# Optimization experiments

Measured on AMD Instinct MI355X. Metric: run time of the kernel, lower is better.

Reference implementation:

```python
import jax, jax.numpy as jnp
import numpy as np

N_NODES = 50000
N_EDGES = 800000
IN_FEAT = 512
OUT_FEAT = 128


def multispike(x):
    return jnp.floor(jnp.clip(4.0 * x, 0.0, 4.0) + 0.5) / 4.0


def setup_inputs() -> dict:
    key = jax.random.key(0)
    k1, k2, k3, k4, k5 = jax.random.split(key, 5)
    feat = jax.random.normal(k1, (N_NODES, IN_FEAT), dtype=jnp.float32)
    # Xavier-uniform-like init for the weight parameter
    limit = np.sqrt(6.0 / (IN_FEAT + OUT_FEAT)).astype(np.float32)
    weight = jax.random.uniform(k2, (IN_FEAT, OUT_FEAT), dtype=jnp.float32,
                                minval=-limit, maxval=limit)
    rows = jnp.sort(jax.random.randint(k3, (N_EDGES,), 0, N_NODES, dtype=jnp.int32))
    cols = jax.random.randint(k4, (N_EDGES,), 0, N_NODES, dtype=jnp.int32)
    edge_weight = jax.random.uniform(k5, (N_EDGES,), dtype=jnp.float32)
    return {"feat": feat, "weight": weight, "rows": rows, "cols": cols,
            "edge_weight": edge_weight}


def reference(feat, weight, rows, cols, edge_weight):
    # x = feat @ W                     [N, out_feat]
    x = jnp.matmul(feat, weight)
    # x = spmm(adj, x): out[i] = sum_{e: rows[e]==i} w_e * x[cols[e]]
    edge_feats = edge_weight[:, None] * x[cols]          # [E, out_feat]
    x = jax.ops.segment_sum(edge_feats, rows, num_segments=N_NODES)
    # quantized multi-spike activation
    return multispike(x)
```

## Files before the change

### kernel.cpp

```cpp
#include <hip/hip_runtime.h>

#define N_NODES 50000
#define N_EDGES 800000
#define IN_FEAT 512
#define OUT_FEAT 128


__device__ __forceinline__ float multispike(float a) {
    return floorf(fminf(fmaxf(4.0f * a, 0.0f), 4.0f) + 0.5f) * 0.25f;
}

__device__ __forceinline__ int bswz(int q) { return q ^ ((q >> 3) & 1); }

__global__ __launch_bounds__(128) void gemm_kernel(const float* __restrict__ A,
                                                   const float* __restrict__ B,
                                                   float* __restrict__ C, int M) {
    __shared__ float As[32][68];
    __shared__ float Bs[32][128];

    const int tid = threadIdx.x;
    const int tx = tid & 15;
    const int ty = tid >> 4;
    const int block_m = blockIdx.x * 64;

    const int bq0 = bswz(2 * tx) * 4;
    const int bq1 = bswz(2 * tx + 1) * 4;

    float acc[8][8];
#pragma unroll
    for (int i = 0; i < 8; i++)
#pragma unroll
        for (int j = 0; j < 8; j++) acc[i][j] = 0.0f;

    for (int k0 = 0; k0 < IN_FEAT; k0 += 32) {
#pragma unroll
        for (int i = 0; i < 4; i++) {
            int f = tid + i * 128;
            int r = f >> 3;
            int kq = (f & 7) << 2;
            int gm = block_m + r;
            float4 v = make_float4(0.f, 0.f, 0.f, 0.f);
            if (gm < M) v = *(const float4*)(A + (size_t)gm * IN_FEAT + k0 + kq);
            As[kq + 0][r] = v.x;
            As[kq + 1][r] = v.y;
            As[kq + 2][r] = v.z;
            As[kq + 3][r] = v.w;
        }
#pragma unroll
        for (int i = 0; i < 8; i++) {
            int f = tid + i * 128;
            int r = f >> 5;
            int q = f & 31;
            *(float4*)&Bs[r][bswz(q) * 4] =
                *(const float4*)(B + (size_t)(k0 + r) * OUT_FEAT + q * 4);
        }
        __syncthreads();

#pragma unroll
        for (int k = 0; k < 32; k++) {
            float4 a0 = *(const float4*)&As[k][ty * 8];
            float4 a1 = *(const float4*)&As[k][ty * 8 + 4];
            float4 b0 = *(const float4*)&Bs[k][bq0];
            float4 b1 = *(const float4*)&Bs[k][bq1];
            float av[8] = {a0.x, a0.y, a0.z, a0.w, a1.x, a1.y, a1.z, a1.w};
            float bv[8] = {b0.x, b0.y, b0.z, b0.w, b1.x, b1.y, b1.z, b1.w};
#pragma unroll
            for (int i = 0; i < 8; i++)
#pragma unroll
                for (int j = 0; j < 8; j++)
                    acc[i][j] = fmaf(av[i], bv[j], acc[i][j]);
        }
        __syncthreads();
    }

#pragma unroll
    for (int i = 0; i < 8; i++) {
        int gm = block_m + ty * 8 + i;
        if (gm < M) {
            float* cp = C + (size_t)gm * OUT_FEAT + tx * 8;
            *(float4*)cp = make_float4(acc[i][0], acc[i][1], acc[i][2], acc[i][3]);
            *(float4*)(cp + 4) = make_float4(acc[i][4], acc[i][5], acc[i][6], acc[i][7]);
        }
    }
}

__global__ __launch_bounds__(256) void rowptr_kernel(const int* __restrict__ rows,
                                                     int* __restrict__ row_ptr) {
    int i = blockIdx.x * blockDim.x + threadIdx.x;
    if (i > N_NODES) return;
    int lo = 0, hi = N_EDGES;
    while (lo < hi) {
        int mid = (lo + hi) >> 1;
        if (rows[mid] < i) lo = mid + 1; else hi = mid;
    }
    row_ptr[i] = lo;
}

__global__ __launch_bounds__(256) void spmm_kernel(const float* __restrict__ x,
                                                   const int* __restrict__ cols,
                                                   const float* __restrict__ ew,
                                                   const int* __restrict__ row_ptr,
                                                   float* __restrict__ out) {
    const int wave = threadIdx.x >> 6;
    const int lane = threadIdx.x & 63;
    const int r = blockIdx.x * 4 + wave;
    if (r >= N_NODES) return;

    const int e0 = row_ptr[r];
    const int e1 = row_ptr[r + 1];
    const float2* __restrict__ x2 = (const float2*)x;

    float accx = 0.0f, accy = 0.0f;
    int e = e0;
    for (; e + 8 <= e1; e += 8) {
        int c[8];
        float w[8];
        float2 v[8];
#pragma unroll
        for (int j = 0; j < 8; j++) {
            c[j] = cols[e + j];
            w[j] = ew[e + j];
        }
#pragma unroll
        for (int j = 0; j < 8; j++) {
            v[j] = x2[(size_t)c[j] * 64 + lane];
        }
#pragma unroll
        for (int j = 0; j < 8; j++) {
            accx = fmaf(w[j], v[j].x, accx);
            accy = fmaf(w[j], v[j].y, accy);
        }
    }
    for (; e < e1; e++) {
        int c = cols[e];
        float w = ew[e];
        float2 v = x2[(size_t)c * 64 + lane];
        accx = fmaf(w, v.x, accx);
        accy = fmaf(w, v.y, accy);
    }
    float2* out2 = (float2*)out;
    out2[(size_t)r * 64 + lane] = make_float2(multispike(accx), multispike(accy));
}

extern "C" void kernel_launch(void* const* d_in, const int* in_sizes, int n_in,
                              void* d_out, int out_size, void* d_ws, size_t ws_size,
                              hipStream_t stream) {
    const float* feat = (const float*)d_in[0];
    const float* weight = (const float*)d_in[1];
    const int* rows = (const int*)d_in[2];
    const int* cols = (const int*)d_in[3];
    const float* ew = (const float*)d_in[4];
    float* out = (float*)d_out;

    float* x = (float*)d_ws;
    int* row_ptr = (int*)((char*)d_ws + (size_t)N_NODES * OUT_FEAT * sizeof(float));

    rowptr_kernel<<<(N_NODES + 256) / 256, 256, 0, stream>>>(rows, row_ptr);
    gemm_kernel<<<(N_NODES + 63) / 64, 128, 0, stream>>>(feat, weight, x, N_NODES);
    spmm_kernel<<<(N_NODES + 3) / 4, 256, 0, stream>>>(x, cols, ew, row_ptr, out);
}
```

Measured before the change: 316.2 us.

## Replace shared-memory tiled GEMM with wave-per-16-rows register GEMM using uniform A loads

Rewrites the dense feat@W GEMM so that each wave computes 16 output rows. Each lane holds two output columns, B is read straight from global memory as float2, and the A row values are wave-uniform float4 loads that can become scalar loads. This removes the shared-memory staging, the transposed stores and the __syncthreads barriers. In exchange B is re-read from L2/L1 by every wave and each FMA has much less register-level reuse than the old 8x8 tile, so the kernel may become bound by load issue or latency.

```diff
diff --git a/kernel.cpp b/kernel.cpp
--- a/kernel.cpp
+++ b/kernel.cpp
@@ -10,77 +10,51 @@
     return floorf(fminf(fmaxf(4.0f * a, 0.0f), 4.0f) + 0.5f) * 0.25f;
 }
 
-__device__ __forceinline__ int bswz(int q) { return q ^ ((q >> 3) & 1); }
-
-__global__ __launch_bounds__(128) void gemm_kernel(const float* __restrict__ A,
+__global__ __launch_bounds__(256) void gemm_kernel(const float* __restrict__ A,
                                                    const float* __restrict__ B,
                                                    float* __restrict__ C, int M) {
-    __shared__ float As[32][68];
-    __shared__ float Bs[32][128];
+    const int lane = threadIdx.x & 63;
+    const int wv = __builtin_amdgcn_readfirstlane(threadIdx.x >> 6);
+    const int row0 = blockIdx.x * 64 + wv * 16;
 
-    const int tid = threadIdx.x;
-    const int tx = tid & 15;
-    const int ty = tid >> 4;
-    const int block_m = blockIdx.x * 64;
+    const float2* __restrict__ B2 = (const float2*)B;
 
-    const int bq0 = bswz(2 * tx) * 4;
-    const int bq1 = bswz(2 * tx + 1) * 4;
-
-    float acc[8][8];
+    const float* Ar[16];
 #pragma unroll
-    for (int i = 0; i < 8; i++)
-#pragma unroll
-        for (int j = 0; j < 8; j++) acc[i][j] = 0.0f;
-
-    for (int k0 = 0; k0 < IN_FEAT; k0 += 32) {
-#pragma unroll
-        for (int i = 0; i < 4; i++) {
-            int f = tid + i * 128;
-            int r = f >> 3;
-            int kq = (f & 7) << 2;
-            int gm = block_m + r;
-            float4 v = make_float4(0.f, 0.f, 0.f, 0.f);
-            if (gm < M) v = *(const float4*)(A + (size_t)gm * IN_FEAT + k0 + kq);
-            As[kq + 0][r] = v.x;
-            As[kq + 1][r] = v.y;
-            As[kq + 2][r] = v.z;
-            As[kq + 3][r] = v.w;
-        }
-#pragma unroll
-        for (int i = 0; i < 8; i++) {
-            int f = tid + i * 128;
-            int r = f >> 5;
-            int q = f & 31;
-            *(float4*)&Bs[r][bswz(q) * 4] =
-                *(const float4*)(B + (size_t)(k0 + r) * OUT_FEAT + q * 4);
-        }
-        __syncthreads();
-
-#pragma unroll
-        for (int k = 0; k < 32; k++) {
-            float4 a0 = *(const float4*)&As[k][ty * 8];
-            float4 a1 = *(const float4*)&As[k][ty * 8 + 4];
-            float4 b0 = *(const float4*)&Bs[k][bq0];
-            float4 b1 = *(const float4*)&Bs[k][bq1];
-            float av[8] = {a0.x, a0.y, a0.z, a0.w, a1.x, a1.y, a1.z, a1.w};
-            float bv[8] = {b0.x, b0.y, b0.z, b0.w, b1.x, b1.y, b1.z, b1.w};
-#pragma unroll
-            for (int i = 0; i < 8; i++)
-#pragma unroll
-                for (int j = 0; j < 8; j++)
-                    acc[i][j] = fmaf(av[i], bv[j], acc[i][j]);
-        }
-        __syncthreads();
+    for (int m = 0; m < 16; m++) {
+        int r = row0 + m;
+        if (r > M - 1) r = M - 1;
+        Ar[m] = A + (size_t)r * IN_FEAT;
     }
 
+    float2 acc[16];
 #pragma unroll
-    for (int i = 0; i < 8; i++) {
-        int gm = block_m + ty * 8 + i;
-        if (gm < M) {
-            float* cp = C + (size_t)gm * OUT_FEAT + tx * 8;
-            *(float4*)cp = make_float4(acc[i][0], acc[i][1], acc[i][2], acc[i][3]);
-            *(float4*)(cp + 4) = make_float4(acc[i][4], acc[i][5], acc[i][6], acc[i][7]);
+    for (int m = 0; m < 16; m++) acc[m] = make_float2(0.f, 0.f);
+
+    for (int k0 = 0; k0 < IN_FEAT; k0 += 4) {
+        float2 b0 = B2[(size_t)(k0 + 0) * 64 + lane];
+        float2 b1 = B2[(size_t)(k0 + 1) * 64 + lane];
+        float2 b2 = B2[(size_t)(k0 + 2) * 64 + lane];
+        float2 b3 = B2[(size_t)(k0 + 3) * 64 + lane];
+#pragma unroll
+        for (int m = 0; m < 16; m++) {
+            float4 a = *(const float4*)(Ar[m] + k0);
+            acc[m].x = fmaf(a.x, b0.x, acc[m].x);
+            acc[m].y = fmaf(a.x, b0.y, acc[m].y);
+            acc[m].x = fmaf(a.y, b1.x, acc[m].x);
+            acc[m].y = fmaf(a.y, b1.y, acc[m].y);
+            acc[m].x = fmaf(a.z, b2.x, acc[m].x);
+            acc[m].y = fmaf(a.z, b2.y, acc[m].y);
+            acc[m].x = fmaf(a.w, b3.x, acc[m].x);
+            acc[m].y = fmaf(a.w, b3.y, acc[m].y);
         }
+    }
+
+    float2* __restrict__ C2 = (float2*)C;
+#pragma unroll
+    for (int m = 0; m < 16; m++) {
+        int r = row0 + m;
+        if (r < M) C2[(size_t)r * 64 + lane] = acc[m];
     }
 }
 
@@ -156,6 +130,6 @@
     int* row_ptr = (int*)((char*)d_ws + (size_t)N_NODES * OUT_FEAT * sizeof(float));
 
     rowptr_kernel<<<(N_NODES + 256) / 256, 256, 0, stream>>>(rows, row_ptr);
-    gemm_kernel<<<(N_NODES + 63) / 64, 128, 0, stream>>>(feat, weight, x, N_NODES);
+    gemm_kernel<<<(N_NODES + 63) / 64, 256, 0, stream>>>(feat, weight, x, N_NODES);
     spmm_kernel<<<(N_NODES + 3) / 4, 256, 0, stream>>>(x, cols, ew, row_ptr, out);
 }
```

After: 515.2 us. 62.9% more time.
